# Kernel tuning notes

Hardware: AMD Instinct MI355X
Metric: run time of the kernel (lower is better)

## Reference

```python
import jax, jax.numpy as jnp
import numpy as np

D_MODEL = 1024
H = 16
BLOCK_SIZE = 64
STRIDE = 64
CAUSAL = False


def create_sparse_mask(T, block_size, stride, causal):
    i = jnp.arange(T)[:, None]
    j = jnp.arange(T)[None, :]
    same_block = (i // block_size) == (j // block_size)
    strided = ((i - j) % stride) == 0
    allow = same_block | strided
    if causal:
        allow = allow & (j <= i)
    return allow  # [T, T] bool


def setup_inputs() -> dict:
    key = jax.random.key(0)
    ks = jax.random.split(key, 7)
    B, T, D = 1, 4096, D_MODEL
    scale = 1.0 / np.sqrt(D)
    return {
        "q": jax.random.normal(ks[0], (B, T, D), jnp.float32),
        "k": jax.random.normal(ks[1], (B, T, D), jnp.float32),
        "v": jax.random.normal(ks[2], (B, T, D), jnp.float32),
        "mask": jnp.ones((B, T, T), dtype=bool),
        "Wq": jax.random.normal(ks[3], (D, D), jnp.float32) * scale,
        "Wk": jax.random.normal(ks[4], (D, D), jnp.float32) * scale,
        "Wv": jax.random.normal(ks[5], (D, D), jnp.float32) * scale,
        "Wo": jax.random.normal(ks[6], (D, D), jnp.float32) * scale,
    }


def reference(q, k, v, mask, Wq, Wk, Wv, Wo):
    # NOTE: the original module computes Q, K, V all from the first arg `q`;
    # k and v inputs are accepted but unused (faithful reproduction).
    B, T, D = q.shape
    h, dk = H, D // H

    def proj(x, W):  # nn.Linear(bias=False): x @ W.T -> [B, h, T, dk]
        return (x @ W.T).reshape(B, T, h, dk).transpose(0, 2, 1, 3)

    qh, kh, vh = proj(q, Wq), proj(q, Wk), proj(q, Wv)

    sparse = create_sparse_mask(T, BLOCK_SIZE, STRIDE, CAUSAL)  # [T, T]
    attn_mask = sparse[None, None, :, :] & mask[:, None, :, :]  # [B, h(broadcast), T, T]

    scores = jnp.einsum("bhqd,bhkd->bhqk", qh, kh) / np.sqrt(dk)
    scores = jnp.where(attn_mask, scores, -jnp.inf)
    attn = jax.nn.softmax(scores, axis=-1)  # dropout p=0.0 -> identity
    out = jnp.einsum("bhqk,bhkd->bhqd", attn, vh)
    out = out.transpose(0, 2, 1, 3).reshape(B, T, D)
    return out @ Wo.T
```

## Files before the change

### kernel.cpp

```cpp
#include <hip/hip_runtime.h>
#include <stdint.h>

typedef __attribute__((ext_vector_type(8))) short bf16x8;
typedef __attribute__((ext_vector_type(4))) float f32x4;
typedef __attribute__((ext_vector_type(4))) unsigned short us4;
typedef __attribute__((ext_vector_type(8))) unsigned short us8;

static __device__ __forceinline__ unsigned short f2bf(float f) {
  unsigned u = __float_as_uint(f);
  u = (u + 0x7FFFu + ((u >> 16) & 1u)) >> 16;
  return (unsigned short)u;
}
static __device__ __forceinline__ float bf2f(unsigned short u) {
  return __uint_as_float(((unsigned)u) << 16);
}

#define MFMA16(a, b, c) __builtin_amdgcn_mfma_f32_16x16x32_bf16((a), (b), (c), 0, 0, 0)

#define GLL16(g, l)                                                             \
  __builtin_amdgcn_global_load_lds(                                             \
      (__attribute__((address_space(1))) unsigned int*)(uintptr_t)(g),          \
      (__attribute__((address_space(3))) unsigned int*)(uintptr_t)(l), 16, 0, 0)

__global__ void prep_kernel(const float* __restrict__ q,
                            const float* __restrict__ Wq,
                            const float* __restrict__ Wk,
                            const float* __restrict__ Wv,
                            const float* __restrict__ Wo,
                            unsigned short* __restrict__ Xb,
                            unsigned short* __restrict__ Wqkv,
                            unsigned short* __restrict__ Wob) {
  const long idx = (long)blockIdx.x * 256 + threadIdx.x;
  const int row = (int)(idx >> 7);
  const int c = (int)(idx & 127) * 8;
  const float* src;
  unsigned short* dst;
  float scale = 1.f;
  if (row < 4096) {
    src = q + (long)row * 1024;
    dst = Xb + (long)row * 1024;
  } else if (row < 7168) {
    const int w = row - 4096;
    src = ((w < 1024) ? Wq : (w < 2048) ? Wk : Wv) + (long)(w & 1023) * 1024;
    dst = Wqkv + (long)w * 1024;
    if (w < 1024) scale = 0.125f;
  } else {
    const int w = row - 7168;
    src = Wo + (long)w * 1024;
    dst = Wob + (long)w * 1024;
  }
  float4 x0 = *(const float4*)(src + c);
  float4 x1 = *(const float4*)(src + c + 4);
  float xs[8] = {x0.x * scale, x0.y * scale, x0.z * scale, x0.w * scale,
                 x1.x * scale, x1.y * scale, x1.z * scale, x1.w * scale};
  us8 hi;
#pragma unroll
  for (int i = 0; i < 8; i++) hi[i] = f2bf(xs[i]);
  *(us8*)(dst + c) = hi;
}

__device__ __forceinline__ void stage_u64(unsigned short* lds_unit,
                                          const unsigned short* g_unit,
                                          int k0, int tid) {
  const int r = tid >> 3;
  const int j = tid & 7;
  const int js = j ^ (r & 7);
  GLL16(g_unit + (size_t)r * 1024 + k0 + js * 8, lds_unit + (tid & ~63) * 8);
}

__global__ __launch_bounds__(512, 2) void gemm_128x192(
    const unsigned short* __restrict__ A, const unsigned short* __restrict__ B,
    unsigned short* __restrict__ C) {
  const int NT = 16;
  __shared__ __align__(16) unsigned short AS[2][8192];
  __shared__ __align__(16) unsigned short BS[2][12288];
  const int wg = blockIdx.x;
  const int swz = (wg & 7) * 64 + (wg >> 3);
  const int bm = swz >> 4, bn = swz & 15;
  const int tid = threadIdx.x;
  const int wave = tid >> 6, lane = tid & 63;
  const int wm = wave >> 2, wn = wave & 3;

  const unsigned short* Ag = A + (size_t)bm * 128 * 1024;
  const unsigned short* Bg = B + (size_t)bn * 192 * 1024;

  f32x4 zero = {0.f, 0.f, 0.f, 0.f};
  f32x4 acc[4][3];
#pragma unroll
  for (int m = 0; m < 4; m++)
#pragma unroll
    for (int n = 0; n < 3; n++) acc[m][n] = zero;

  stage_u64(AS[0], Ag, 0, tid);
  stage_u64(AS[0] + 4096, Ag + 64 * 1024, 0, tid);
  stage_u64(BS[0], Bg, 0, tid);
  stage_u64(BS[0] + 4096, Bg + 64 * 1024, 0, tid);
  stage_u64(BS[0] + 8192, Bg + 128 * 1024, 0, tid);
  stage_u64(BS[1], Bg, 64, tid);
  stage_u64(BS[1] + 4096, Bg + 64 * 1024, 64, tid);
  stage_u64(BS[1] + 8192, Bg + 128 * 1024, 64, tid);
  stage_u64(AS[1], Ag, 64, tid);
  asm volatile("s_waitcnt vmcnt(4)" ::: "memory");
  __builtin_amdgcn_s_barrier();

  const int fr = lane & 15;
  const int fko = (lane >> 4) * 8;

  for (int t = 0; t < NT; t++) {
    const int cur = t & 1;
    const unsigned short* At = AS[cur];
    const unsigned short* Bt = BS[cur];
    bf16x8 av[4][2], bv[3][2];

#pragma unroll
    for (int m = 0; m < 4; m++) {
      const int row = wm * 64 + m * 16 + fr;
      const int sw = (row & 7) << 3;
      av[m][0] = *(const bf16x8*)&At[row * 64 + (fko ^ sw)];
      av[m][1] = *(const bf16x8*)&At[row * 64 + ((32 + fko) ^ sw)];
    }
#pragma unroll
    for (int n = 0; n < 2; n++) {
      const int row = wn * 48 + n * 16 + fr;
      const int sw = (row & 7) << 3;
      bv[n][0] = *(const bf16x8*)&Bt[row * 64 + (fko ^ sw)];
      bv[n][1] = *(const bf16x8*)&Bt[row * 64 + ((32 + fko) ^ sw)];
    }
    if (t + 1 < NT) stage_u64(AS[cur ^ 1] + 4096, Ag + 64 * 1024, (t + 1) * 64, tid);
    __builtin_amdgcn_s_barrier();
    __builtin_amdgcn_s_setprio(1);
#pragma unroll
    for (int m = 0; m < 4; m++)
#pragma unroll
      for (int n = 0; n < 2; n++) {
        acc[m][n] = MFMA16(av[m][0], bv[n][0], acc[m][n]);
        acc[m][n] = MFMA16(av[m][1], bv[n][1], acc[m][n]);
      }
    __builtin_amdgcn_s_setprio(0);
    __builtin_amdgcn_s_barrier();

    {
      const int row = wn * 48 + 32 + fr;
      const int sw = (row & 7) << 3;
      bv[2][0] = *(const bf16x8*)&Bt[row * 64 + (fko ^ sw)];
      bv[2][1] = *(const bf16x8*)&Bt[row * 64 + ((32 + fko) ^ sw)];
    }
    if (t + 2 < NT) stage_u64(AS[cur], Ag, (t + 2) * 64, tid);
    __builtin_amdgcn_s_barrier();
    __builtin_amdgcn_s_setprio(1);
#pragma unroll
    for (int m = 0; m < 4; m++) {
      acc[m][2] = MFMA16(av[m][0], bv[2][0], acc[m][2]);
      acc[m][2] = MFMA16(av[m][1], bv[2][1], acc[m][2]);
    }
    __builtin_amdgcn_s_setprio(0);
    __builtin_amdgcn_s_barrier();

    if (t + 2 < NT) {
      stage_u64(BS[cur], Bg, (t + 2) * 64, tid);
      stage_u64(BS[cur] + 4096, Bg + 64 * 1024, (t + 2) * 64, tid);
      stage_u64(BS[cur] + 8192, Bg + 128 * 1024, (t + 2) * 64, tid);
    }
    if (t < NT - 1) {
      if (t + 2 < NT)
        asm volatile("s_waitcnt vmcnt(4)" ::: "memory");
      else
        asm volatile("s_waitcnt vmcnt(0)" ::: "memory");
      __builtin_amdgcn_s_barrier();
    }
  }

  const int crow = bm * 128 + wm * 64 + (lane >> 4) * 4;
  const int ccol = bn * 192 + wn * 48 + (lane & 15);
#pragma unroll
  for (int m = 0; m < 4; m++)
#pragma unroll
    for (int n = 0; n < 3; n++)
#pragma unroll
      for (int r = 0; r < 4; r++)
        C[(size_t)(crow + m * 16 + r) * 3072 + ccol + n * 16] =
            f2bf(acc[m][n][r]);
}

__global__ __launch_bounds__(256) void attn_kernel(
    const unsigned short* __restrict__ QKV, unsigned short* __restrict__ O0,
    unsigned short* __restrict__ O1, float2* __restrict__ St0,
    float2* __restrict__ St1) {
  __shared__ __align__(16) unsigned short QP[64 * 64];
  __shared__ __align__(16) unsigned short Ks[64 * 64];
  __shared__ __align__(16) unsigned short Vt[64 * 64];
  __shared__ __align__(16) float Sf[64 * 68];
  const int bid = blockIdx.x;
  const int f = bid >> 10, h = (bid >> 6) & 15, t = bid & 63;
  const int tid = threadIdx.x;
  const int wave = tid >> 6, lane = tid & 63;

  {
#pragma unroll
    for (int i = 0; i < 2; i++) {
      const int c = i * 256 + tid;
      const int row = c >> 3;
      const int ch = c & 7;
      const int js = ch ^ (row & 7);
      const long grow = f ? ((long)row * 64 + t) : ((long)t * 64 + row);
      const unsigned short* gq = QKV + grow * 3072 + h * 64 + js * 8;
      const int ldof = i * 2048 + (wave << 9);
      GLL16(gq, QP + ldof);
      GLL16(gq + 1024, Ks + ldof);
    }
  }
  {
    const int j = tid >> 2;
    const int d0 = (tid & 3) * 16;
    const long grow = f ? ((long)j * 64 + t) : ((long)t * 64 + j);
    const unsigned short* vsrc = QKV + grow * 3072 + 2048 + h * 64 + d0;
#pragma unroll
    for (int e = 0; e < 16; e += 8) {
      bf16x8 v8 = *(const bf16x8*)(vsrc + e);
#pragma unroll
      for (int c = 0; c < 8; c++) {
        const int d = d0 + e + c;
        Vt[d * 64 + (j ^ ((d & 7) << 3))] = (unsigned short)v8[c];
      }
    }
  }
  __syncthreads();

  const int wr = wave >> 1, wc = wave & 1;
  const int fr = lane & 15;
  const int fko = (lane >> 4) * 8;
  f32x4 zero = {0.f, 0.f, 0.f, 0.f};

  {
    f32x4 acc[2][2] = {{zero, zero}, {zero, zero}};
#pragma unroll
    for (int s = 0; s < 2; s++) {
      bf16x8 av[2], bv[2];
#pragma unroll
      for (int m = 0; m < 2; m++) {
        const int row = wr * 32 + m * 16 + fr;
        const int kk = (s * 32 + fko) ^ ((row & 7) << 3);
        av[m] = *(const bf16x8*)&QP[row * 64 + kk];
      }
#pragma unroll
      for (int n = 0; n < 2; n++) {
        const int row = wc * 32 + n * 16 + fr;
        const int kk = (s * 32 + fko) ^ ((row & 7) << 3);
        bv[n] = *(const bf16x8*)&Ks[row * 64 + kk];
      }
#pragma unroll
      for (int m = 0; m < 2; m++)
#pragma unroll
        for (int n = 0; n < 2; n++) acc[m][n] = MFMA16(av[m], bv[n], acc[m][n]);
    }
    const int r0 = wr * 32 + (lane >> 4) * 4;
    const int c0 = wc * 32 + (lane & 15);
#pragma unroll
    for (int m = 0; m < 2; m++)
#pragma unroll
      for (int n = 0; n < 2; n++)
#pragma unroll
        for (int r = 0; r < 4; r++)
          Sf[(r0 + m * 16 + r) * 68 + c0 + n * 16] = acc[m][n][r];
  }
  __syncthreads();

  {
    const int qrow = tid >> 2;
    const int sub = tid & 3;
    float s[16];
#pragma unroll
    for (int e = 0; e < 4; e++) {
      float4 v = *(const float4*)&Sf[qrow * 68 + sub * 16 + e * 4];
      s[e * 4 + 0] = v.x;
      s[e * 4 + 1] = v.y;
      s[e * 4 + 2] = v.z;
      s[e * 4 + 3] = v.w;
    }
    float mx = s[0];
#pragma unroll
    for (int e = 1; e < 16; e++) mx = fmaxf(mx, s[e]);
    mx = fmaxf(mx, __shfl_xor(mx, 1, 64));
    mx = fmaxf(mx, __shfl_xor(mx, 2, 64));
    float ev[16];
    float z = 0.f;
#pragma unroll
    for (int e = 0; e < 16; e++) {
      float v = __expf(s[e] - mx);
      if (f == 1 && (sub * 16 + e) == qrow) v = 0.f;
      ev[e] = v;
      z += v;
    }
    z += __shfl_xor(z, 1, 64);
    z += __shfl_xor(z, 2, 64);
    const float inv = 1.f / z;
    __attribute__((aligned(16))) unsigned short pb[16];
#pragma unroll
    for (int e = 0; e < 16; e++) pb[e] = f2bf(ev[e] * inv);
#pragma unroll
    for (int cc = 0; cc < 2; cc++) {
      const int chunk = (sub * 2 + cc) ^ (qrow & 7);
      *(us8*)&QP[qrow * 64 + chunk * 8] = *(const us8*)&pb[cc * 8];
    }
    if (sub == 0) {
      const long qg = f ? ((long)qrow * 64 + t) : ((long)t * 64 + qrow);
      (f ? St1 : St0)[(long)h * 4096 + qg] = make_float2(mx, z);
    }
  }
  __syncthreads();

  f32x4 acc[2][2] = {{zero, zero}, {zero, zero}};
#pragma unroll
  for (int s = 0; s < 2; s++) {
    bf16x8 av[2], bv[2];
#pragma unroll
    for (int m = 0; m < 2; m++) {
      const int row = wr * 32 + m * 16 + fr;
      const int kk = (s * 32 + fko) ^ ((row & 7) << 3);
      av[m] = *(const bf16x8*)&QP[row * 64 + kk];
    }
#pragma unroll
    for (int n = 0; n < 2; n++) {
      const int row = wc * 32 + n * 16 + fr;
      const int kk = (s * 32 + fko) ^ ((row & 7) << 3);
      bv[n] = *(const bf16x8*)&Vt[row * 64 + kk];
    }
#pragma unroll
    for (int m = 0; m < 2; m++)
#pragma unroll
      for (int n = 0; n < 2; n++) acc[m][n] = MFMA16(av[m], bv[n], acc[m][n]);
  }
  const int r0 = wr * 32 + (lane >> 4) * 4;
  const int c0 = wc * 32 + (lane & 15);
  if (f == 0) {
#pragma unroll
    for (int m = 0; m < 2; m++)
#pragma unroll
      for (int n = 0; n < 2; n++)
#pragma unroll
        for (int r = 0; r < 4; r++)
          O0[((long)t * 64 + r0 + m * 16 + r) * 1024 + h * 64 + c0 + n * 16] =
              f2bf(acc[m][n][r]);
  } else {
#pragma unroll
    for (int m = 0; m < 2; m++)
#pragma unroll
      for (int n = 0; n < 2; n++)
#pragma unroll
        for (int r = 0; r < 4; r++)
          O1[(((long)h * 64 + t) * 64 + r0 + m * 16 + r) * 64 + c0 + n * 16] =
              f2bf(acc[m][n][r]);
  }
}

__global__ void combine_kernel(const unsigned short* __restrict__ O0,
                               const unsigned short* __restrict__ O1,
                               const float2* __restrict__ St0,
                               const float2* __restrict__ St1,
                               unsigned short* __restrict__ Ot) {
  const int i = blockIdx.x;
  const int c = threadIdx.x * 4;
  const int h = c >> 6, d = c & 63, b = i >> 6, r = i & 63;
  us4 n0 = *(const us4*)(O0 + (long)i * 1024 + c);
  us4 n1 = *(const us4*)(O1 + (((long)h * 64 + r) * 64 + b) * 64 + d);
  float2 s0 = St0[(long)h * 4096 + i];
  float2 s1 = St1[(long)h * 4096 + i];
  const float M = fmaxf(s0.x, s1.x);
  const float w0 = __expf(s0.x - M) * s0.y;
  const float w1 = __expf(s1.x - M) * s1.y;
  const float inv = 1.f / (w0 + w1);
  const float a0 = w0 * inv, a1 = w1 * inv;
  us4 hi;
#pragma unroll
  for (int e = 0; e < 4; e++)
    hi[e] = f2bf(a0 * bf2f(n0[e]) + a1 * bf2f(n1[e]));
  *(us4*)(Ot + (long)i * 1024 + c) = hi;
}

__device__ __forceinline__ void stage_rows64(unsigned short* lds,
                                             const unsigned short* g, int K,
                                             int k0, int tid) {
#pragma unroll
  for (int i = 0; i < 2; i++) {
    const int c = i * 256 + tid;
    const int r = c >> 3, j = c & 7;
    const int js = j ^ (r & 7);
    GLL16(g + (size_t)r * K + k0 + js * 8, lds + (i * 256 + (tid & ~63)) * 8);
  }
}

__global__ __launch_bounds__(256) void gemm_bt_64x128(
    const unsigned short* __restrict__ A, const unsigned short* __restrict__ B,
    float* __restrict__ C, int K, int N) {
  __shared__ __align__(16) unsigned short As[64 * 64];
  __shared__ __align__(16) unsigned short Bs[128 * 64];
  const int bm = blockIdx.x, bn = blockIdx.y;
  const int tid = threadIdx.x;
  const int wave = tid >> 6, lane = tid & 63;
  const int wr = wave >> 1, wc = wave & 1;

  f32x4 zero = {0.f, 0.f, 0.f, 0.f};
  f32x4 acc[2][4];
#pragma unroll
  for (int m = 0; m < 2; m++)
#pragma unroll
    for (int n = 0; n < 4; n++) acc[m][n] = zero;

  const unsigned short* Ab = A + (size_t)bm * 64 * K;
  const unsigned short* Bb = B + (size_t)bn * 128 * K;

  const int fr = lane & 15;
  const int fko = (lane >> 4) * 8;

  for (int k0 = 0; k0 < K; k0 += 64) {
    if (k0) __syncthreads();
    stage_rows64(As, Ab, K, k0, tid);
    stage_rows64(Bs, Bb, K, k0, tid);
    stage_rows64(Bs + 4096, Bb + (size_t)64 * K, K, k0, tid);
    __syncthreads();
    bf16x8 af[2][2], bv[4][2];
#pragma unroll
    for (int m = 0; m < 2; m++) {
      const int row = wr * 32 + m * 16 + fr;
      const int sw = (row & 7) << 3;
      af[m][0] = *(const bf16x8*)&As[row * 64 + (fko ^ sw)];
      af[m][1] = *(const bf16x8*)&As[row * 64 + ((32 + fko) ^ sw)];
    }
#pragma unroll
    for (int n = 0; n < 4; n++) {
      const int row = wc * 64 + n * 16 + fr;
      const int sw = (row & 7) << 3;
      bv[n][0] = *(const bf16x8*)&Bs[row * 64 + (fko ^ sw)];
      bv[n][1] = *(const bf16x8*)&Bs[row * 64 + ((32 + fko) ^ sw)];
    }
#pragma unroll
    for (int m = 0; m < 2; m++)
#pragma unroll
      for (int n = 0; n < 4; n++) {
        acc[m][n] = MFMA16(af[m][0], bv[n][0], acc[m][n]);
        acc[m][n] = MFMA16(af[m][1], bv[n][1], acc[m][n]);
      }
  }

  const int crow = bm * 64 + wr * 32 + (lane >> 4) * 4;
  const int ccol = bn * 128 + wc * 64 + (lane & 15);
#pragma unroll
  for (int m = 0; m < 2; m++)
#pragma unroll
    for (int n = 0; n < 4; n++)
#pragma unroll
      for (int r = 0; r < 4; r++)
        C[(size_t)(crow + m * 16 + r) * N + ccol + n * 16] = acc[m][n][r];
}

extern "C" void kernel_launch(void* const* d_in, const int* in_sizes, int n_in,
                              void* d_out, int out_size, void* d_ws,
                              size_t ws_size, hipStream_t stream) {
  const float* q = (const float*)d_in[0];
  const float* Wq = (const float*)d_in[4];
  const float* Wk = (const float*)d_in[5];
  const float* Wv = (const float*)d_in[6];
  const float* Wo = (const float*)d_in[7];
  float* out = (float*)d_out;

  char* ws = (char*)d_ws;
  unsigned short* Xb = (unsigned short*)(ws);
  unsigned short* Ot = (unsigned short*)(ws);
  unsigned short* Wqkv = (unsigned short*)(ws + 8388608);
  unsigned short* Wob = (unsigned short*)(ws + 14680064);
  unsigned short* QKVb = (unsigned short*)(ws + 16777216);
  unsigned short* O0 = (unsigned short*)(ws + 41943040);
  unsigned short* O1 = (unsigned short*)(ws + 50331648);
  float2* St0 = (float2*)(ws + 58720256);
  float2* St1 = (float2*)(ws + 59244544);

  prep_kernel<<<4096, 256, 0, stream>>>(q, Wq, Wk, Wv, Wo, Xb, Wqkv, Wob);

  gemm_128x192<<<512, 512, 0, stream>>>(Xb, Wqkv, QKVb);

  attn_kernel<<<2048, 256, 0, stream>>>(QKVb, O0, O1, St0, St1);
  combine_kernel<<<4096, 256, 0, stream>>>(O0, O1, St0, St1, Ot);

  gemm_bt_64x128<<<dim3(64, 8), 256, 0, stream>>>(Ot, Wob, out, 1024, 1024);
}
```

Baseline: 78.88 us.

## Fuse split-attention combine into output projection GEMM A-tile loading

Removes the separate combine kernel and the bf16 Ot round trip. The output projection GEMM now loads both partial attention outputs and their softmax statistics directly, merges them in registers, and writes the merged A tile into LDS. The next K-slice's partials are prefetched into registers, overlapping those loads with MFMA work. In exchange, every one of the 8 column-block workgroups recomputes the merge for the same rows, which duplicates global reads of O0, O1 and the stats, and the A path no longer uses async global-to-LDS loads.

```diff
diff --git a/kernel.cpp b/kernel.cpp
--- a/kernel.cpp
+++ b/kernel.cpp
@@ -353,30 +353,6 @@
   }
 }
 
-__global__ void combine_kernel(const unsigned short* __restrict__ O0,
-                               const unsigned short* __restrict__ O1,
-                               const float2* __restrict__ St0,
-                               const float2* __restrict__ St1,
-                               unsigned short* __restrict__ Ot) {
-  const int i = blockIdx.x;
-  const int c = threadIdx.x * 4;
-  const int h = c >> 6, d = c & 63, b = i >> 6, r = i & 63;
-  us4 n0 = *(const us4*)(O0 + (long)i * 1024 + c);
-  us4 n1 = *(const us4*)(O1 + (((long)h * 64 + r) * 64 + b) * 64 + d);
-  float2 s0 = St0[(long)h * 4096 + i];
-  float2 s1 = St1[(long)h * 4096 + i];
-  const float M = fmaxf(s0.x, s1.x);
-  const float w0 = __expf(s0.x - M) * s0.y;
-  const float w1 = __expf(s1.x - M) * s1.y;
-  const float inv = 1.f / (w0 + w1);
-  const float a0 = w0 * inv, a1 = w1 * inv;
-  us4 hi;
-#pragma unroll
-  for (int e = 0; e < 4; e++)
-    hi[e] = f2bf(a0 * bf2f(n0[e]) + a1 * bf2f(n1[e]));
-  *(us4*)(Ot + (long)i * 1024 + c) = hi;
-}
-
 __device__ __forceinline__ void stage_rows64(unsigned short* lds,
                                              const unsigned short* g, int K,
                                              int k0, int tid) {
@@ -389,9 +365,10 @@
   }
 }
 
-__global__ __launch_bounds__(256) void gemm_bt_64x128(
-    const unsigned short* __restrict__ A, const unsigned short* __restrict__ B,
-    float* __restrict__ C, int K, int N) {
+__global__ __launch_bounds__(256) void out_gemm_fused(
+    const unsigned short* __restrict__ O0, const unsigned short* __restrict__ O1,
+    const float2* __restrict__ St0, const float2* __restrict__ St1,
+    const unsigned short* __restrict__ Bw, float* __restrict__ C) {
   __shared__ __align__(16) unsigned short As[64 * 64];
   __shared__ __align__(16) unsigned short Bs[128 * 64];
   const int bm = blockIdx.x, bn = blockIdx.y;
@@ -406,18 +383,69 @@
 #pragma unroll
     for (int n = 0; n < 4; n++) acc[m][n] = zero;
 
-  const unsigned short* Ab = A + (size_t)bm * 64 * K;
-  const unsigned short* Bb = B + (size_t)bn * 128 * K;
+  int rr[2], dd[2], cc[2];
+#pragma unroll
+  for (int i = 0; i < 2; i++) {
+    const int c = i * 256 + tid;
+    const int r = c >> 3, j = c & 7;
+    rr[i] = r;
+    dd[i] = (j ^ (r & 7)) * 8;
+    cc[i] = c;
+  }
+  const unsigned short* Bb = Bw + (size_t)bn * 128 * 1024;
+
+  us8 o0r[2], o1r[2], am[2];
+  float2 s0r[2], s1r[2];
+
+#define LOADA(hh)                                                          \
+  {                                                                        \
+    const int h_ = (hh);                                                   \
+    __attribute__((unused)) int dummy;                                     \
+    {                                                                      \
+      const long gi0 = (long)bm * 64 + rr[0];                              \
+      o0r[0] = *(const us8*)&O0[gi0 * 1024 + h_ * 64 + dd[0]];             \
+      o1r[0] = *(const us8*)&O1[(((long)h_ * 64 + (gi0 & 63)) * 64 +       \
+                                 (gi0 >> 6)) * 64 + dd[0]];                \
+      s0r[0] = St0[(long)h_ * 4096 + gi0];                                 \
+      s1r[0] = St1[(long)h_ * 4096 + gi0];                                 \
+      const long gi1 = (long)bm * 64 + rr[1];                              \
+      o0r[1] = *(const us8*)&O0[gi1 * 1024 + h_ * 64 + dd[1]];             \
+      o1r[1] = *(const us8*)&O1[(((long)h_ * 64 + (gi1 & 63)) * 64 +       \
+                                 (gi1 >> 6)) * 64 + dd[1]];                \
+      s0r[1] = St0[(long)h_ * 4096 + gi1];                                 \
+      s1r[1] = St1[(long)h_ * 4096 + gi1];                                 \
+    }                                                                      \
+  }
+
+#define MERGEA()                                                           \
+  {                                                                        \
+    _Pragma("unroll") for (int i_ = 0; i_ < 2; i_++) {                     \
+      const float M_ = fmaxf(s0r[i_].x, s1r[i_].x);                        \
+      const float w0_ = __expf(s0r[i_].x - M_) * s0r[i_].y;                \
+      const float w1_ = __expf(s1r[i_].x - M_) * s1r[i_].y;                \
+      const float inv_ = 1.f / (w0_ + w1_);                                \
+      const float a0_ = w0_ * inv_, a1_ = w1_ * inv_;                      \
+      us8 v_;                                                              \
+      _Pragma("unroll") for (int e_ = 0; e_ < 8; e_++)                     \
+          v_[e_] = f2bf(a0_ * bf2f(o0r[i_][e_]) + a1_ * bf2f(o1r[i_][e_]));\
+      am[i_] = v_;                                                         \
+    }                                                                      \
+  }
+
+  LOADA(0);
+  MERGEA();
+  *(us8*)&As[cc[0] * 8] = am[0];
+  *(us8*)&As[cc[1] * 8] = am[1];
+  stage_rows64(Bs, Bb, 1024, 0, tid);
+  stage_rows64(Bs + 4096, Bb + (size_t)64 * 1024, 1024, 0, tid);
+  LOADA(1);
+  __syncthreads();
+  MERGEA();
 
   const int fr = lane & 15;
   const int fko = (lane >> 4) * 8;
 
-  for (int k0 = 0; k0 < K; k0 += 64) {
-    if (k0) __syncthreads();
-    stage_rows64(As, Ab, K, k0, tid);
-    stage_rows64(Bs, Bb, K, k0, tid);
-    stage_rows64(Bs + 4096, Bb + (size_t)64 * K, K, k0, tid);
-    __syncthreads();
+  for (int t = 0; t < 16; t++) {
     bf16x8 af[2][2], bv[4][2];
 #pragma unroll
     for (int m = 0; m < 2; m++) {
@@ -440,6 +468,16 @@
         acc[m][n] = MFMA16(af[m][0], bv[n][0], acc[m][n]);
         acc[m][n] = MFMA16(af[m][1], bv[n][1], acc[m][n]);
       }
+    if (t < 15) {
+      __syncthreads();
+      *(us8*)&As[cc[0] * 8] = am[0];
+      *(us8*)&As[cc[1] * 8] = am[1];
+      stage_rows64(Bs, Bb, 1024, (t + 1) * 64, tid);
+      stage_rows64(Bs + 4096, Bb + (size_t)64 * 1024, 1024, (t + 1) * 64, tid);
+      if (t + 1 < 15) LOADA(t + 2);
+      __syncthreads();
+      if (t + 1 < 15) MERGEA();
+    }
   }
 
   const int crow = bm * 64 + wr * 32 + (lane >> 4) * 4;
@@ -450,7 +488,7 @@
     for (int n = 0; n < 4; n++)
 #pragma unroll
       for (int r = 0; r < 4; r++)
-        C[(size_t)(crow + m * 16 + r) * N + ccol + n * 16] = acc[m][n][r];
+        C[(size_t)(crow + m * 16 + r) * 1024 + ccol + n * 16] = acc[m][n][r];
 }
 
 extern "C" void kernel_launch(void* const* d_in, const int* in_sizes, int n_in,
@@ -465,7 +503,6 @@
 
   char* ws = (char*)d_ws;
   unsigned short* Xb = (unsigned short*)(ws);
-  unsigned short* Ot = (unsigned short*)(ws);
   unsigned short* Wqkv = (unsigned short*)(ws + 8388608);
   unsigned short* Wob = (unsigned short*)(ws + 14680064);
   unsigned short* QKVb = (unsigned short*)(ws + 16777216);
@@ -479,7 +516,6 @@
   gemm_128x192<<<512, 512, 0, stream>>>(Xb, Wqkv, QKVb);
 
   attn_kernel<<<2048, 256, 0, stream>>>(QKVb, O0, O1, St0, St1);
-  combine_kernel<<<4096, 256, 0, stream>>>(O0, O1, St0, St1, Ot);
-
-  gemm_bt_64x128<<<dim3(64, 8), 256, 0, stream>>>(Ot, Wob, out, 1024, 1024);
-}
+
+  out_gemm_fused<<<dim3(64, 8), 256, 0, stream>>>(O0, O1, St0, St1, Wob, out);
+}
```

Result: slower. 87.41 us (+10.8%).
